# Kernel optimization log

Hardware: AMD Instinct MI355X
Metric: run time of the kernel (lower is better)

## Reference

```python
import jax, jax.numpy as jnp
import numpy as np

N = 100_000      # nodes
E = 1_600_000    # edges (avg degree 16)
H = 128          # hidden_dim
L = 2            # num_layers
G = 64           # graphs in batch
BN_EPS = 1e-5


def setup_inputs() -> dict:
    key = jax.random.key(0)
    ks = jax.random.split(key, 20)
    x = jax.random.normal(ks[0], (N, 1), jnp.float32)
    edge_index = jax.random.randint(ks[1], (2, E), 0, N, dtype=jnp.int64)
    edge_attr = jax.random.uniform(ks[2], (E, 1), jnp.float32)
    batch = jnp.sort(jax.random.randint(ks[3], (N,), 0, G, dtype=jnp.int64))
    s = 1.0 / np.sqrt(H)
    return {
        "x": x, "edge_index": edge_index, "edge_attr": edge_attr, "batch": batch,
        "enc_w": jax.random.normal(ks[4], (1, H), jnp.float32),
        "enc_b": jnp.zeros((H,), jnp.float32),
        "eenc_w": jax.random.normal(ks[5], (1, H), jnp.float32),
        "eenc_b": jnp.zeros((H,), jnp.float32),
        "eps": jnp.zeros((L,), jnp.float32),  # train_eps=True, init 0
        "w1": jax.random.normal(ks[6], (L, H, H), jnp.float32) * s,
        "b1": jnp.zeros((L, H), jnp.float32),
        "w2": jax.random.normal(ks[7], (L, H, H), jnp.float32) * s,
        "b2": jnp.zeros((L, H), jnp.float32),
        "gamma": jnp.ones((L, H), jnp.float32),
        "beta": jnp.zeros((L, H), jnp.float32),
        "cw1": jax.random.normal(ks[8], (H, H // 2), jnp.float32) * s,
        "cb1": jnp.zeros((H // 2,), jnp.float32),
        "cw2": jax.random.normal(ks[9], (H // 2, 1), jnp.float32) * (1.0 / np.sqrt(H // 2)),
        "cb2": jnp.zeros((1,), jnp.float32),
    }


def reference(x, edge_index, edge_attr, batch,
              enc_w, enc_b, eenc_w, eenc_b,
              eps, w1, b1, w2, b2, gamma, beta,
              cw1, cb1, cw2, cb2):
    # Inference mode: dropout = identity, BatchNorm uses running stats (mean=0, var=1).
    h = x @ enc_w + enc_b                 # [N, H] node encoder
    ea = edge_attr @ eenc_w + eenc_b      # [E, H] edge encoder
    src, dst = edge_index[0], edge_index[1]
    inv_std = 1.0 / jnp.sqrt(1.0 + BN_EPS)
    for l in range(L):
        # GINEConv: out = MLP((1+eps)*x + sum_j relu(x_j + e_ij))
        msg = jax.nn.relu(h[src] + ea)                         # [E, H] gather + fuse
        agg = jax.ops.segment_sum(msg, dst, num_segments=N)    # [N, H] scatter-sum
        z = (1.0 + eps[l]) * h + agg
        z = jax.nn.relu(z @ w1[l] + b1[l]) @ w2[l] + b2[l]      # GIN MLP
        h = jax.nn.relu(gamma[l] * z * inv_std + beta[l])       # BN (eval) + ReLU
    # global mean pool over graphs
    cnt = jax.ops.segment_sum(jnp.ones((N, 1), h.dtype), batch, num_segments=G)
    pooled = jax.ops.segment_sum(h, batch, num_segments=G) / jnp.maximum(cnt, 1.0)
    hc = jax.nn.relu(pooled @ cw1 + cb1)
    out = jax.nn.sigmoid(hc @ cw2 + cb2)
    return out.squeeze(-1)                # [G]
```

## Files before the change

kernel.cpp:

```cpp
#include <hip/hip_runtime.h>

#define HDIM 128
#define NGRAPH 64
#define INVSTD 0.99999500003749972f
#define WTPAD 136
#define WSLOT (128 * WTPAD)

typedef unsigned short ushort_t;
typedef unsigned int uint_t;
typedef unsigned char uchar_t;
typedef __attribute__((ext_vector_type(8))) short bf16x8;
typedef __attribute__((ext_vector_type(4))) float f32x4;
typedef __attribute__((ext_vector_type(2))) float f32x2;

__device__ __forceinline__ float bf2f(uint_t u) {
    return __int_as_float((int)(u << 16));
}
__device__ __forceinline__ float bf2f_hi(uint_t u) {
    return __int_as_float((int)(u & 0xFFFF0000u));
}
__device__ __forceinline__ uint_t f2bf(float f) {
    uint_t x = __float_as_uint(f);
    return (x + 0x7FFFu + ((x >> 16) & 1u)) >> 16;
}
__device__ __forceinline__ uint_t pack2(float a, float b) {
    return f2bf(a) | (f2bf(b) << 16);
}
__device__ __forceinline__ uint_t pack4fp8(float a, float b, float c, float d) {
    int v = __builtin_amdgcn_cvt_pk_fp8_f32(a, b, 0, false);
    v = __builtin_amdgcn_cvt_pk_fp8_f32(c, d, v, true);
    return (uint_t)v;
}

__global__ void k_encode(const float* __restrict__ x, const float* __restrict__ ew,
                         const float* __restrict__ enb, const float* __restrict__ ebe,
                         ushort_t* __restrict__ hb, uchar_t* __restrict__ hq, int N) {
    int tid = blockIdx.x * blockDim.x + threadIdx.x;
    int stride = gridDim.x * blockDim.x;
    int q = tid & 15;
    float4 wa = ((const float4*)ew)[2 * q];
    float4 wb = ((const float4*)ew)[2 * q + 1];
    float4 ba = ((const float4*)enb)[2 * q];
    float4 bb = ((const float4*)enb)[2 * q + 1];
    float4 ea = ((const float4*)ebe)[2 * q];
    float4 eb2 = ((const float4*)ebe)[2 * q + 1];
    ba.x += ea.x; ba.y += ea.y; ba.z += ea.z; ba.w += ea.w;
    bb.x += eb2.x; bb.y += eb2.y; bb.z += eb2.z; bb.w += eb2.w;
    int total = N * 16;
    for (int t = tid; t < total; t += stride) {
        int n = t >> 4;
        float xv = x[n];
        float v0 = fmaf(xv, wa.x, ba.x), v1 = fmaf(xv, wa.y, ba.y);
        float v2 = fmaf(xv, wa.z, ba.z), v3 = fmaf(xv, wa.w, ba.w);
        float v4 = fmaf(xv, wb.x, bb.x), v5 = fmaf(xv, wb.y, bb.y);
        float v6 = fmaf(xv, wb.z, bb.z), v7 = fmaf(xv, wb.w, bb.w);
        uint4 o;
        o.x = pack2(v0, v1); o.y = pack2(v2, v3);
        o.z = pack2(v4, v5); o.w = pack2(v6, v7);
        ((uint4*)(hb + (size_t)n * HDIM))[q] = o;
        uint2 o8;
        o8.x = pack4fp8(v0, v1, v2, v3);
        o8.y = pack4fp8(v4, v5, v6, v7);
        ((uint2*)(hq + (size_t)n * HDIM))[q] = o8;
    }
}

__global__ void k_prepw(const float* __restrict__ w1, const float* __restrict__ w2,
                        ushort_t* __restrict__ wtg) {
    int t = blockIdx.x * 256 + threadIdx.x;
    if (t >= 4 * 16384) return;
    int w = t >> 14, idx = t & 16383;
    int k = idx >> 7, n = idx & 127;
    const float* src = ((w & 1) ? w2 : w1) + (size_t)(w >> 1) * 16384;
    wtg[(size_t)w * WSLOT + n * WTPAD + k] = (ushort_t)f2bf(src[idx]);
}

__global__ void k_hist(const int* __restrict__ ei, int* deg, int* __restrict__ rank_, int E) {
    int e = blockIdx.x * 256 + threadIdx.x;
    if (e < E) {
        int d = ei[E + e];
        rank_[e] = atomicAdd(&deg[d], 1);
    }
}

__global__ void k_scan1(const int* __restrict__ deg, int* rs, int* bsum, int N) {
    __shared__ int sm[256];
    int gid = blockIdx.x * 256 + threadIdx.x;
    int v = (gid < N) ? deg[gid] : 0;
    sm[threadIdx.x] = v;
    __syncthreads();
    #pragma unroll
    for (int off = 1; off < 256; off <<= 1) {
        int t = (threadIdx.x >= off) ? sm[threadIdx.x - off] : 0;
        __syncthreads();
        sm[threadIdx.x] += t;
        __syncthreads();
    }
    if (gid < N) rs[gid] = sm[threadIdx.x] - v;
    if (threadIdx.x == 255) bsum[blockIdx.x] = sm[255];
}

__global__ void k_scan2(int* bsum, int nb) {
    __shared__ int sm[512];
    int t = threadIdx.x;
    int v = (t < nb) ? bsum[t] : 0;
    sm[t] = v;
    __syncthreads();
    #pragma unroll
    for (int off = 1; off < 512; off <<= 1) {
        int u = (t >= off) ? sm[t - off] : 0;
        __syncthreads();
        sm[t] += u;
        __syncthreads();
    }
    if (t < nb) bsum[t] = sm[t] - v;
}

__global__ void k_scan3(int* rs, const int* __restrict__ bsum, int N, int E) {
    int gid = blockIdx.x * 256 + threadIdx.x;
    if (gid < N) rs[gid] += bsum[gid >> 8];
    if (gid == N) rs[N] = E;
}

__global__ void k_scatter(const int* __restrict__ ei, const float* __restrict__ attr,
                          const int* __restrict__ rs, const int* __restrict__ rank_,
                          int2* __restrict__ epack, int E) {
    int e = blockIdx.x * 256 + threadIdx.x;
    if (e < E) {
        int s = ei[e], d = ei[E + e];
        int p = rs[d] + rank_[e];
        epack[p] = make_int2(s, __float_as_int(attr[e]));
    }
}

__device__ __forceinline__ void acc_edge(float acc[8], const uint2& u, float at,
        const float4& wa, const float4& wb) {
    f32x2 p0 = __builtin_amdgcn_cvt_pk_f32_fp8(u.x, false);
    f32x2 p1 = __builtin_amdgcn_cvt_pk_f32_fp8(u.x, true);
    f32x2 p2 = __builtin_amdgcn_cvt_pk_f32_fp8(u.y, false);
    f32x2 p3 = __builtin_amdgcn_cvt_pk_f32_fp8(u.y, true);
    acc[0] += fmaxf(fmaf(at, wa.x, p0[0]), 0.f);
    acc[1] += fmaxf(fmaf(at, wa.y, p0[1]), 0.f);
    acc[2] += fmaxf(fmaf(at, wa.z, p1[0]), 0.f);
    acc[3] += fmaxf(fmaf(at, wa.w, p1[1]), 0.f);
    acc[4] += fmaxf(fmaf(at, wb.x, p2[0]), 0.f);
    acc[5] += fmaxf(fmaf(at, wb.y, p2[1]), 0.f);
    acc[6] += fmaxf(fmaf(at, wb.z, p3[0]), 0.f);
    acc[7] += fmaxf(fmaf(at, wb.w, p3[1]), 0.f);
}

__global__ __launch_bounds__(256) void k_agg(
    const uchar_t* __restrict__ hq, const ushort_t* __restrict__ hb,
    const int* __restrict__ rs, const int2* __restrict__ epack,
    const float* __restrict__ ew, const float* __restrict__ ebv,
    const float* __restrict__ epsp, ushort_t* __restrict__ zb, int N) {
    int wave = (blockIdx.x * 256 + threadIdx.x) >> 6;
    if (wave >= N) return;
    int lane = threadIdx.x & 63;
    int p = lane >> 4;
    int q = lane & 15;
    int n = wave;
    int beg = rs[n];
    int cntE = rs[n + 1] - beg;
    float4 wa = ((const float4*)ew)[2 * q], wb = ((const float4*)ew)[2 * q + 1];

    float acc[8] = {0.f, 0.f, 0.f, 0.f, 0.f, 0.f, 0.f, 0.f};
    float acc2[8] = {0.f, 0.f, 0.f, 0.f, 0.f, 0.f, 0.f, 0.f};
    int j = p;
    for (; j + 4 < cntE; j += 8) {
        int2 e1 = epack[beg + j];
        int2 e2 = epack[beg + j + 4];
        uint2 u1 = *(const uint2*)(hq + (size_t)e1.x * HDIM + q * 8);
        uint2 u2 = *(const uint2*)(hq + (size_t)e2.x * HDIM + q * 8);
        acc_edge(acc,  u1, __int_as_float(e1.y), wa, wb);
        acc_edge(acc2, u2, __int_as_float(e2.y), wa, wb);
    }
    if (j < cntE) {
        int2 e1 = epack[beg + j];
        uint2 u1 = *(const uint2*)(hq + (size_t)e1.x * HDIM + q * 8);
        acc_edge(acc, u1, __int_as_float(e1.y), wa, wb);
    }
    #pragma unroll
    for (int k = 0; k < 8; ++k) {
        float v = acc[k] + acc2[k];
        v += __shfl_xor(v, 16);
        v += __shfl_xor(v, 32);
        acc[k] = v;
    }
    if (p == 0) {
        float sc = 1.f + epsp[0];
        float4 ba = ((const float4*)ebv)[2 * q], bb = ((const float4*)ebv)[2 * q + 1];
        float s0 = sc * ba.x, s1 = sc * ba.y, s2 = sc * ba.z, s3 = sc * ba.w;
        float s4 = sc * bb.x, s5 = sc * bb.y, s6 = sc * bb.z, s7 = sc * bb.w;
        uint4 u = *(const uint4*)(hb + (size_t)n * HDIM + q * 8);
        uint4 ob;
        ob.x = pack2(fmaf(sc, bf2f(u.x & 0xFFFFu), acc[0]) - s0,
                     fmaf(sc, bf2f_hi(u.x),        acc[1]) - s1);
        ob.y = pack2(fmaf(sc, bf2f(u.y & 0xFFFFu), acc[2]) - s2,
                     fmaf(sc, bf2f_hi(u.y),        acc[3]) - s3);
        ob.z = pack2(fmaf(sc, bf2f(u.z & 0xFFFFu), acc[4]) - s4,
                     fmaf(sc, bf2f_hi(u.z),        acc[5]) - s5);
        ob.w = pack2(fmaf(sc, bf2f(u.w & 0xFFFFu), acc[6]) - s6,
                     fmaf(sc, bf2f_hi(u.w),        acc[7]) - s7);
        *(uint4*)(zb + (size_t)n * HDIM + q * 8) = ob;
    }
}

template<int MODE, int EBF, int WQ>
__global__ __launch_bounds__(256) void k_gemm(
    const ushort_t* __restrict__ A, const ushort_t* __restrict__ WT,
    const float* __restrict__ bias, const float* __restrict__ gam,
    const float* __restrict__ bet, const float* __restrict__ ebe,
    ushort_t* __restrict__ out, uchar_t* __restrict__ outq, int N) {
    __shared__ ushort_t wt[128 * WTPAD];
    int tid = threadIdx.x;
    #pragma unroll
    for (int i = 0; i < 9; ++i) {
        int c = i * 256 + tid;
        if (c < 2176) ((bf16x8*)wt)[c] = ((const bf16x8*)WT)[c];
    }
    __syncthreads();

    int wid = tid >> 6, lane = tid & 63;
    int ra = lane & 15, qa = lane >> 4;

    bf16x8 bfr[4][8];
    #pragma unroll
    for (int ks = 0; ks < 4; ++ks)
        #pragma unroll
        for (int nf = 0; nf < 8; ++nf)
            bfr[ks][nf] = *(const bf16x8*)&wt[(nf * 16 + ra) * WTPAD + ks * 32 + qa * 8];

    float bi[8], gg[8], be_[8], ef[8];
    #pragma unroll
    for (int nf = 0; nf < 8; ++nf) {
        int col = nf * 16 + ra;
        bi[nf] = bias[col];
        if (MODE == 1) { gg[nf] = gam[col]; be_[nf] = bet[col]; }
        if (EBF)       { ef[nf] = ebe[col]; }
    }

    bf16x8 azero;
    #pragma unroll
    for (int j = 0; j < 8; ++j) azero[j] = 0;

    #pragma unroll
    for (int it = 0; it < 4; ++it) {
        int m0 = blockIdx.x * 256 + it * 64 + wid * 16;
        int mr = m0 + ra;
        bf16x8 afr[4];
        #pragma unroll
        for (int ks = 0; ks < 4; ++ks)
            afr[ks] = (mr < N) ? *(const bf16x8*)&A[(size_t)mr * HDIM + ks * 32 + qa * 8]
                               : azero;
        f32x4 acc[8];
        #pragma unroll
        for (int nf = 0; nf < 8; ++nf)
            #pragma unroll
            for (int j = 0; j < 4; ++j) acc[nf][j] = 0.f;
        #pragma unroll
        for (int ks = 0; ks < 4; ++ks)
            #pragma unroll
            for (int nf = 0; nf < 8; ++nf)
                acc[nf] = __builtin_amdgcn_mfma_f32_16x16x32_bf16(afr[ks], bfr[ks][nf], acc[nf], 0, 0, 0);
        #pragma unroll
        for (int nf = 0; nf < 8; ++nf) {
            #pragma unroll
            for (int r = 0; r < 4; ++r) {
                int row = m0 + qa * 4 + r;
                if (row < N) {
                    float v = acc[nf][r] + bi[nf];
                    if (MODE == 0) v = fmaxf(v, 0.f);
                    else           v = fmaxf(fmaf(gg[nf] * v, INVSTD, be_[nf]), 0.f);
                    if (EBF)       v += ef[nf];
                    out[(size_t)row * HDIM + nf * 16 + ra] = (ushort_t)f2bf(v);
                    if (WQ)
                        outq[(size_t)row * HDIM + nf * 16 + ra] =
                            (uchar_t)(__builtin_amdgcn_cvt_pk_fp8_f32(v, 0.f, 0, false) & 0xFF);
                }
            }
        }
    }
}

#define PCHUNK 256
#define PWIN 4
__global__ __launch_bounds__(256) void k_pool2(const ushort_t* __restrict__ hb,
                                               const int* __restrict__ batch,
                                               float* pooled, int N) {
    __shared__ float acc[PWIN][HDIM];
    int n0 = blockIdx.x * PCHUNK;
    if (n0 >= N) return;
    int n1 = min(n0 + PCHUNK, N);
    int g0 = batch[n0];
    int g1 = batch[n1 - 1];
    for (int i = threadIdx.x; i < PWIN * HDIM; i += 256) ((float*)acc)[i] = 0.f;
    __syncthreads();

    int grp = threadIdx.x >> 5;
    int q = threadIdx.x & 31;
    float4 racc = make_float4(0.f, 0.f, 0.f, 0.f);
    int gcur = g0;
    for (int n = n0 + grp; n < n1; n += 8) {
        int g = batch[n];
        if (g != gcur) {
            int w = gcur - g0;
            float* p = (w < PWIN) ? &acc[w][q * 4] : (pooled + gcur * HDIM + q * 4);
            atomicAdd(p + 0, racc.x); atomicAdd(p + 1, racc.y);
            atomicAdd(p + 2, racc.z); atomicAdd(p + 3, racc.w);
            racc = make_float4(0.f, 0.f, 0.f, 0.f);
            gcur = g;
        }
        uint2 u = ((const uint2*)(hb + (size_t)n * HDIM))[q];
        racc.x += bf2f(u.x);
        racc.y += bf2f_hi(u.x);
        racc.z += bf2f(u.y);
        racc.w += bf2f_hi(u.y);
    }
    {
        int w = gcur - g0;
        float* p = (w < PWIN) ? &acc[w][q * 4] : (pooled + gcur * HDIM + q * 4);
        atomicAdd(p + 0, racc.x); atomicAdd(p + 1, racc.y);
        atomicAdd(p + 2, racc.z); atomicAdd(p + 3, racc.w);
    }
    __syncthreads();

    int span = min(g1 - g0 + 1, PWIN);
    for (int i = threadIdx.x; i < span * HDIM; i += 256) {
        int w = i >> 7, f = i & 127;
        float v = acc[w][f];
        if (v != 0.f) atomicAdd(pooled + (g0 + w) * HDIM + f, v);
    }
}

__global__ void k_classify(const float* __restrict__ pooled, const int* __restrict__ batch,
                           const float* __restrict__ cw1, const float* __restrict__ cb1,
                           const float* __restrict__ cw2, const float* __restrict__ cb2,
                           float* __restrict__ out, int N) {
    __shared__ float p[HDIM];
    int g = blockIdx.x, j = threadIdx.x;
    int lo = 0, hi = N;
    while (lo < hi) { int m = (lo + hi) >> 1; if (batch[m] < g) lo = m + 1; else hi = m; }
    int lo2 = lo, hi2 = N;
    while (lo2 < hi2) { int m = (lo2 + hi2) >> 1; if (batch[m] < g + 1) lo2 = m + 1; else hi2 = m; }
    float c = fmaxf((float)(lo2 - lo), 1.f);
    p[j]      = pooled[g * HDIM + j] / c;
    p[j + 64] = pooled[g * HDIM + j + 64] / c;
    __syncthreads();
    float acc = cb1[j];
    #pragma unroll 4
    for (int k = 0; k < HDIM; ++k) acc = fmaf(p[k], cw1[k * 64 + j], acc);
    acc = fmaxf(acc, 0.f);
    float v = acc * cw2[j];
    #pragma unroll
    for (int off = 32; off > 0; off >>= 1) v += __shfl_down(v, off, 64);
    if (j == 0) out[g] = 1.f / (1.f + expf(-(v + cb2[0])));
}

static inline size_t align_up(size_t v, size_t a) { return (v + a - 1) & ~(a - 1); }

extern "C" void kernel_launch(void* const* d_in, const int* in_sizes, int n_in,
                              void* d_out, int out_size, void* d_ws, size_t ws_size,
                              hipStream_t stream) {
    const float* x      = (const float*)d_in[0];
    const int*   ei     = (const int*)d_in[1];
    const float* eattr  = (const float*)d_in[2];
    const int*   batch  = (const int*)d_in[3];
    const float* enc_w  = (const float*)d_in[4];
    const float* enc_b  = (const float*)d_in[5];
    const float* eenc_w = (const float*)d_in[6];
    const float* eenc_b = (const float*)d_in[7];
    const float* eps    = (const float*)d_in[8];
    const float* w1     = (const float*)d_in[9];
    const float* b1     = (const float*)d_in[10];
    const float* w2     = (const float*)d_in[11];
    const float* b2     = (const float*)d_in[12];
    const float* gamma  = (const float*)d_in[13];
    const float* beta   = (const float*)d_in[14];
    const float* cw1    = (const float*)d_in[15];
    const float* cb1    = (const float*)d_in[16];
    const float* cw2    = (const float*)d_in[17];
    const float* cb2    = (const float*)d_in[18];

    int N = in_sizes[0];
    int E = in_sizes[2];

    char* wsb = (char*)d_ws;
    size_t off = 0;
    ushort_t* hb  = (ushort_t*)(wsb + off); off = align_up(off + (size_t)N * HDIM * 2, 256);
    uchar_t*  hq  = (uchar_t*)(wsb + off);  off = align_up(off + (size_t)N * HDIM, 256);
    ushort_t* zb  = (ushort_t*)(wsb + off); off = align_up(off + (size_t)N * HDIM * 2, 256);
    ushort_t* wtg = (ushort_t*)(wsb + off); off = align_up(off + (size_t)4 * WSLOT * 2, 256);
    float* pooled = (float*)(wsb + off);    off = align_up(off + NGRAPH * HDIM * 4, 256);
    int*   deg    = (int*)(wsb + off);      off = align_up(off + (size_t)N * 4, 256);
    int*   rs     = (int*)(wsb + off);      off = align_up(off + (size_t)(N + 1) * 4, 256);
    int*   rank_  = (int*)(wsb + off);      off = align_up(off + (size_t)E * 4, 256);
    int*   bsum   = (int*)(wsb + off);      off = align_up(off + 2048 * 4, 256);
    int2*  epack  = (int2*)(wsb + off);     off = align_up(off + (size_t)E * 8, 256);

    int nb = (N + 255) / 256;
    int eb_blocks = (E + 255) / 256;

    hipMemsetAsync(deg, 0, (size_t)N * 4, stream);
    k_hist<<<eb_blocks, 256, 0, stream>>>(ei, deg, rank_, E);
    k_prepw<<<256, 256, 0, stream>>>(w1, w2, wtg);
    k_scan1<<<nb, 256, 0, stream>>>(deg, rs, bsum, N);
    k_scan2<<<1, 512, 0, stream>>>(bsum, nb);
    k_scan3<<<(N + 256) / 256, 256, 0, stream>>>(rs, bsum, N, E);
    k_scatter<<<eb_blocks, 256, 0, stream>>>(ei, eattr, rs, rank_, epack, E);

    hipMemsetAsync(pooled, 0, NGRAPH * HDIM * sizeof(float), stream);
    k_encode<<<2048, 256, 0, stream>>>(x, enc_w, enc_b, eenc_b, hb, hq, N);

    int gblocks = (N + 255) / 256;
    int ablocks = (N * 64 + 255) / 256;

    k_agg<<<ablocks, 256, 0, stream>>>(hq, hb, rs, epack, eenc_w, eenc_b, eps + 0, zb, N);
    k_gemm<0,0,0><<<gblocks, 256, 0, stream>>>(zb, wtg + 0 * WSLOT, b1, nullptr, nullptr,
                                               nullptr, zb, nullptr, N);
    k_gemm<1,1,1><<<gblocks, 256, 0, stream>>>(zb, wtg + 1 * WSLOT, b2, gamma, beta,
                                               eenc_b, hb, hq, N);
    k_agg<<<ablocks, 256, 0, stream>>>(hq, hb, rs, epack, eenc_w, eenc_b, eps + 1, zb, N);
    k_gemm<0,0,0><<<gblocks, 256, 0, stream>>>(zb, wtg + 2 * WSLOT, b1 + HDIM, nullptr, nullptr,
                                               nullptr, zb, nullptr, N);
    k_gemm<1,0,0><<<gblocks, 256, 0, stream>>>(zb, wtg + 3 * WSLOT, b2 + HDIM, gamma + HDIM,
                                               beta + HDIM, nullptr, hb, nullptr, N);

    k_pool2<<<(N + PCHUNK - 1) / PCHUNK, 256, 0, stream>>>(hb, batch, pooled, N);
    k_classify<<<NGRAPH, 64, 0, stream>>>(pooled, batch, cw1, cb1, cw2, cb2, (float*)d_out, N);
}
```

Baseline: 330.1 us.

## Replace global-atomic CSR build with two-pass bucketed counting sort

Builds the destination-sorted edge list with a two-level counting sort instead of per-edge global atomics followed by a multi-kernel scan and a random scatter. Edges are first binned into 512-node buckets using shared-memory histograms and then sorted within each bucket in LDS. The aim is to cut global atomic contention and scattered writes. In exchange it adds an intermediate 16-byte-per-edge buffer and one extra pass over the edges, and edge order within a node becomes nondeterministic.

```diff
diff --git a/kernel.cpp b/kernel.cpp
--- a/kernel.cpp
+++ b/kernel.cpp
@@ -5,6 +5,8 @@
 #define INVSTD 0.99999500003749972f
 #define WTPAD 136
 #define WSLOT (128 * WTPAD)
+#define BKN 512
+#define EPB 4096
 
 typedef unsigned short ushort_t;
 typedef unsigned int uint_t;
@@ -75,61 +77,107 @@
     wtg[(size_t)w * WSLOT + n * WTPAD + k] = (ushort_t)f2bf(src[idx]);
 }
 
-__global__ void k_hist(const int* __restrict__ ei, int* deg, int* __restrict__ rank_, int E) {
-    int e = blockIdx.x * 256 + threadIdx.x;
-    if (e < E) {
-        int d = ei[E + e];
-        rank_[e] = atomicAdd(&deg[d], 1);
-    }
-}
-
-__global__ void k_scan1(const int* __restrict__ deg, int* rs, int* bsum, int N) {
+__global__ __launch_bounds__(256) void k_cnt(const int* __restrict__ ei, int* __restrict__ btot,
+                                             int nb, int E) {
+    __shared__ int hist[256];
+    hist[threadIdx.x] = 0;
+    __syncthreads();
+    int e0 = blockIdx.x * EPB;
+    for (int i = threadIdx.x; i < EPB; i += 256) {
+        int e = e0 + i;
+        if (e < E) atomicAdd(&hist[ei[E + e] / BKN], 1);
+    }
+    __syncthreads();
+    int c = hist[threadIdx.x];
+    if (threadIdx.x < nb && c > 0) atomicAdd(&btot[threadIdx.x], c);
+}
+
+__global__ void k_bscan(const int* __restrict__ btot, int* __restrict__ segs, int nb, int E) {
     __shared__ int sm[256];
-    int gid = blockIdx.x * 256 + threadIdx.x;
-    int v = (gid < N) ? deg[gid] : 0;
-    sm[threadIdx.x] = v;
+    int t = threadIdx.x;
+    int v = (t < nb) ? btot[t] : 0;
+    sm[t] = v;
     __syncthreads();
     #pragma unroll
     for (int off = 1; off < 256; off <<= 1) {
-        int t = (threadIdx.x >= off) ? sm[threadIdx.x - off] : 0;
-        __syncthreads();
-        sm[threadIdx.x] += t;
-        __syncthreads();
-    }
-    if (gid < N) rs[gid] = sm[threadIdx.x] - v;
-    if (threadIdx.x == 255) bsum[blockIdx.x] = sm[255];
-}
-
-__global__ void k_scan2(int* bsum, int nb) {
-    __shared__ int sm[512];
-    int t = threadIdx.x;
-    int v = (t < nb) ? bsum[t] : 0;
-    sm[t] = v;
-    __syncthreads();
-    #pragma unroll
-    for (int off = 1; off < 512; off <<= 1) {
         int u = (t >= off) ? sm[t - off] : 0;
         __syncthreads();
         sm[t] += u;
         __syncthreads();
     }
-    if (t < nb) bsum[t] = sm[t] - v;
-}
-
-__global__ void k_scan3(int* rs, const int* __restrict__ bsum, int N, int E) {
-    int gid = blockIdx.x * 256 + threadIdx.x;
-    if (gid < N) rs[gid] += bsum[gid >> 8];
-    if (gid == N) rs[N] = E;
-}
-
-__global__ void k_scatter(const int* __restrict__ ei, const float* __restrict__ attr,
-                          const int* __restrict__ rs, const int* __restrict__ rank_,
-                          int2* __restrict__ epack, int E) {
-    int e = blockIdx.x * 256 + threadIdx.x;
-    if (e < E) {
-        int s = ei[e], d = ei[E + e];
-        int p = rs[d] + rank_[e];
-        epack[p] = make_int2(s, __float_as_int(attr[e]));
+    if (t < nb) segs[t] = sm[t] - v;
+    if (t == 0) segs[nb] = E;
+}
+
+__global__ __launch_bounds__(256) void k_place0(const int* __restrict__ ei,
+                                                const float* __restrict__ attr,
+                                                const int* __restrict__ segs, int* cursor,
+                                                int4* __restrict__ ebuf, int nb, int E) {
+    __shared__ int hist[256];
+    __shared__ int basev[256];
+    hist[threadIdx.x] = 0;
+    __syncthreads();
+    int e0 = blockIdx.x * EPB;
+    for (int i = threadIdx.x; i < EPB; i += 256) {
+        int e = e0 + i;
+        if (e < E) atomicAdd(&hist[ei[E + e] / BKN], 1);
+    }
+    __syncthreads();
+    {
+        int c = hist[threadIdx.x];
+        basev[threadIdx.x] = (threadIdx.x < nb && c > 0) ? atomicAdd(&cursor[threadIdx.x], c) : 0;
+        hist[threadIdx.x] = 0;
+    }
+    __syncthreads();
+    for (int i = threadIdx.x; i < EPB; i += 256) {
+        int e = e0 + i;
+        if (e < E) {
+            int s = ei[e], d = ei[E + e];
+            float a = attr[e];
+            int b = d / BKN;
+            int r = atomicAdd(&hist[b], 1);
+            ebuf[segs[b] + basev[b] + r] = make_int4(s, __float_as_int(a), d, 0);
+        }
+    }
+}
+
+__global__ __launch_bounds__(256) void k_fine(const int4* __restrict__ ebuf,
+                                              const int* __restrict__ segs,
+                                              int2* __restrict__ epack, int* __restrict__ rs,
+                                              int nb, int N, int E) {
+    __shared__ int hist[BKN];
+    __shared__ int cur[BKN];
+    __shared__ int psum[256];
+    int b = blockIdx.x;
+    int d0 = b * BKN;
+    int nd = min(BKN, N - d0);
+    for (int i = threadIdx.x; i < BKN; i += 256) hist[i] = 0;
+    __syncthreads();
+    int s0 = segs[b], s1 = segs[b + 1];
+    for (int e = s0 + threadIdx.x; e < s1; e += 256)
+        atomicAdd(&hist[ebuf[e].z - d0], 1);
+    __syncthreads();
+    int h0 = hist[2 * threadIdx.x], h1 = hist[2 * threadIdx.x + 1];
+    psum[threadIdx.x] = h0 + h1;
+    __syncthreads();
+    #pragma unroll
+    for (int off = 1; off < 256; off <<= 1) {
+        int u = (threadIdx.x >= off) ? psum[threadIdx.x - off] : 0;
+        __syncthreads();
+        psum[threadIdx.x] += u;
+        __syncthreads();
+    }
+    int pb = psum[threadIdx.x] - (h0 + h1);
+    cur[2 * threadIdx.x] = pb;
+    cur[2 * threadIdx.x + 1] = pb + h0;
+    __syncthreads();
+    for (int i = threadIdx.x; i < nd; i += 256) rs[d0 + i] = s0 + cur[i];
+    if (b == nb - 1 && threadIdx.x == 0) rs[N] = E;
+    __syncthreads();
+    for (int e = s0 + threadIdx.x; e < s1; e += 256) {
+        int4 rec = ebuf[e];
+        int r = atomicAdd(&cur[rec.z - d0], 1);
+        epack[s0 + r] = make_int2(rec.x, rec.y);
     }
 }
 
@@ -385,6 +433,9 @@
     int N = in_sizes[0];
     int E = in_sizes[2];
 
+    int nb = (N + BKN - 1) / BKN;
+    int nblk = (E + EPB - 1) / EPB;
+
     char* wsb = (char*)d_ws;
     size_t off = 0;
     ushort_t* hb  = (ushort_t*)(wsb + off); off = align_up(off + (size_t)N * HDIM * 2, 256);
@@ -392,22 +443,20 @@
     ushort_t* zb  = (ushort_t*)(wsb + off); off = align_up(off + (size_t)N * HDIM * 2, 256);
     ushort_t* wtg = (ushort_t*)(wsb + off); off = align_up(off + (size_t)4 * WSLOT * 2, 256);
     float* pooled = (float*)(wsb + off);    off = align_up(off + NGRAPH * HDIM * 4, 256);
-    int*   deg    = (int*)(wsb + off);      off = align_up(off + (size_t)N * 4, 256);
+    int*   btot   = (int*)(wsb + off);      off = align_up(off + (size_t)(nb + 1) * 4, 256);
+    int*   segs   = (int*)(wsb + off);      off = align_up(off + (size_t)(nb + 1) * 4, 256);
+    int*   cursor = (int*)(wsb + off);      off = align_up(off + (size_t)nb * 4, 256);
     int*   rs     = (int*)(wsb + off);      off = align_up(off + (size_t)(N + 1) * 4, 256);
-    int*   rank_  = (int*)(wsb + off);      off = align_up(off + (size_t)E * 4, 256);
-    int*   bsum   = (int*)(wsb + off);      off = align_up(off + 2048 * 4, 256);
+    int4*  ebuf   = (int4*)(wsb + off);     off = align_up(off + (size_t)E * 16, 256);
     int2*  epack  = (int2*)(wsb + off);     off = align_up(off + (size_t)E * 8, 256);
 
-    int nb = (N + 255) / 256;
-    int eb_blocks = (E + 255) / 256;
-
-    hipMemsetAsync(deg, 0, (size_t)N * 4, stream);
-    k_hist<<<eb_blocks, 256, 0, stream>>>(ei, deg, rank_, E);
+    hipMemsetAsync(btot, 0, (size_t)(nb + 1) * 4, stream);
+    hipMemsetAsync(cursor, 0, (size_t)nb * 4, stream);
+    k_cnt<<<nblk, 256, 0, stream>>>(ei, btot, nb, E);
     k_prepw<<<256, 256, 0, stream>>>(w1, w2, wtg);
-    k_scan1<<<nb, 256, 0, stream>>>(deg, rs, bsum, N);
-    k_scan2<<<1, 512, 0, stream>>>(bsum, nb);
-    k_scan3<<<(N + 256) / 256, 256, 0, stream>>>(rs, bsum, N, E);
-    k_scatter<<<eb_blocks, 256, 0, stream>>>(ei, eattr, rs, rank_, epack, E);
+    k_bscan<<<1, 256, 0, stream>>>(btot, segs, nb, E);
+    k_place0<<<nblk, 256, 0, stream>>>(ei, eattr, segs, cursor, ebuf, nb, E);
+    k_fine<<<nb, 256, 0, stream>>>(ebuf, segs, epack, rs, nb, N, E);
 
     hipMemsetAsync(pooled, 0, NGRAPH * HDIM * sizeof(float), stream);
     k_encode<<<2048, 256, 0, stream>>>(x, enc_w, enc_b, eenc_b, hb, hq, N);
```

Result: faster. 302.9 us (-8.2%).
